# Optimization experiments

Measured on AMD Instinct MI355X. Metric: run time of the kernel, lower is better.

The kernel has to match this reference:

```python
import jax, jax.numpy as jnp
import numpy as np


def _ln(x, g, b, eps=1e-5):
    m = jnp.mean(x, axis=-1, keepdims=True)
    v = jnp.mean((x - m) ** 2, axis=-1, keepdims=True)
    return (x - m) / jnp.sqrt(v + eps) * g + b


def _win_part(x, ws):
    # (B,H,W,C) -> (B*nW, ws*ws, C)
    B, H, W, C = x.shape
    x = x.reshape(B, H // ws, ws, W // ws, ws, C)
    x = jnp.transpose(x, (0, 1, 3, 2, 4, 5))
    return x.reshape(-1, ws * ws, C)


def _win_rev(w, ws, H, W):
    # (B*nW, ws, ws, C) -> (B,H,W,C)
    C = w.shape[-1]
    B = w.shape[0] // ((H // ws) * (W // ws))
    x = w.reshape(B, H // ws, W // ws, ws, ws, C)
    x = jnp.transpose(x, (0, 1, 3, 2, 4, 5))
    return x.reshape(B, H, W, C)


def _build_mask(H, W, ws, ss):
    # standard Swin SW-MSA mask, built with numpy at trace time (static shapes)
    img = np.zeros((H, W), np.float32)
    cnt = 0
    for hs in (slice(0, -ws), slice(-ws, -ss), slice(-ss, None)):
        for wsl in (slice(0, -ws), slice(-ws, -ss), slice(-ss, None)):
            img[hs, wsl] = cnt
            cnt += 1
    mw = img.reshape(H // ws, ws, W // ws, ws).transpose(0, 2, 1, 3).reshape(-1, ws * ws)
    diff = mw[:, None, :] - mw[:, :, None]  # (nW, N, N)
    return jnp.asarray(np.where(diff != 0, -np.inf, 0.0).astype(np.float32))


def _swin_block(x, H, W, ws, shift, heads, p):
    B, L, C = x.shape
    hd = C // heads
    N = ws * ws
    shortcut = x
    xg = _ln(x, p['ln1_g'], p['ln1_b']).reshape(B, H, W, C)
    mask = None
    if shift > 0:
        xg = jnp.roll(xg, shift=(-shift, -shift), axis=(1, 2))
        mask = _build_mask(H, W, ws, shift)
    xw = _win_part(xg, ws)  # (B_, N, C)
    qkv = xw @ p['qkv_w'] + p['qkv_b']  # (B_, N, 3C)
    qkv = jnp.transpose(qkv.reshape(-1, N, 3, heads, hd), (2, 0, 3, 1, 4))
    q, k, v = qkv[0] * (hd ** -0.5), qkv[1], qkv[2]  # (B_, h, N, hd)
    attn = jnp.einsum('bhnd,bhmd->bhnm', q, k)
    if mask is not None:
        nW = mask.shape[0]
        attn = attn.reshape(B, nW, heads, N, N) + mask[None, :, None]
        attn = attn.reshape(-1, heads, N, N)
    attn = jax.nn.softmax(attn, axis=-1)
    out = jnp.einsum('bhnm,bhmd->bhnd', attn, v)
    out = jnp.transpose(out, (0, 2, 1, 3)).reshape(-1, N, C)
    out = out @ p['proj_w'] + p['proj_b']
    xg = _win_rev(out.reshape(-1, ws, ws, C), ws, H, W)
    if shift > 0:
        xg = jnp.roll(xg, shift=(shift, shift), axis=(1, 2))
    x = shortcut + xg.reshape(B, L, C)
    h = jax.nn.gelu(_ln(x, p['ln2_g'], p['ln2_b']) @ p['fc1_w'] + p['fc1_b'], approximate=False)
    return x + (h @ p['fc2_w'] + p['fc2_b'])


def _patch_merge(x, H, W, g, b, w):
    B, L, C = x.shape
    xg = x.reshape(B, H, W, C)
    xc = jnp.concatenate([xg[:, 0::2, 0::2], xg[:, 1::2, 0::2], xg[:, 0::2, 1::2], xg[:, 1::2, 1::2]], axis=-1)
    xc = xc.reshape(B, (H // 2) * (W // 2), 4 * C)
    return _ln(xc, g, b) @ w


def setup_inputs() -> dict:
    key = jax.random.key(0)
    ks = jax.random.split(key, 16)
    B, H, W, C = 8, 96, 96, 128
    s = 0.02
    d = {'x': jax.random.normal(ks[0], (B, H * W, C), jnp.float32)}
    i = 1
    for pre in ('a_', 'b_'):
        d[pre + 'ln1_g'] = jnp.ones((C,), jnp.float32)
        d[pre + 'ln1_b'] = jnp.zeros((C,), jnp.float32)
        d[pre + 'qkv_w'] = s * jax.random.normal(ks[i], (C, 3 * C), jnp.float32); i += 1
        d[pre + 'qkv_b'] = jnp.zeros((3 * C,), jnp.float32)
        d[pre + 'proj_w'] = s * jax.random.normal(ks[i], (C, C), jnp.float32); i += 1
        d[pre + 'proj_b'] = jnp.zeros((C,), jnp.float32)
        d[pre + 'ln2_g'] = jnp.ones((C,), jnp.float32)
        d[pre + 'ln2_b'] = jnp.zeros((C,), jnp.float32)
        d[pre + 'fc1_w'] = s * jax.random.normal(ks[i], (C, 4 * C), jnp.float32); i += 1
        d[pre + 'fc1_b'] = jnp.zeros((4 * C,), jnp.float32)
        d[pre + 'fc2_w'] = s * jax.random.normal(ks[i], (4 * C, C), jnp.float32); i += 1
        d[pre + 'fc2_b'] = jnp.zeros((C,), jnp.float32)
    d['mln_g'] = jnp.ones((4 * C,), jnp.float32)
    d['mln_b'] = jnp.zeros((4 * C,), jnp.float32)
    d['red_w'] = s * jax.random.normal(ks[i], (4 * C, 2 * C), jnp.float32)
    d['H'] = H
    d['W'] = W
    return d


def reference(x, a_ln1_g, a_ln1_b, a_qkv_w, a_qkv_b, a_proj_w, a_proj_b, a_ln2_g, a_ln2_b, a_fc1_w, a_fc1_b, a_fc2_w, a_fc2_b, b_ln1_g, b_ln1_b, b_qkv_w, b_qkv_b, b_proj_w, b_proj_b, b_ln2_g, b_ln2_b, b_fc1_w, b_fc1_b, b_fc2_w, b_fc2_b, mln_g, mln_b, red_w, H, W):
    heads, ws = 4, 8
    pa = dict(ln1_g=a_ln1_g, ln1_b=a_ln1_b, qkv_w=a_qkv_w, qkv_b=a_qkv_b, proj_w=a_proj_w, proj_b=a_proj_b, ln2_g=a_ln2_g, ln2_b=a_ln2_b, fc1_w=a_fc1_w, fc1_b=a_fc1_b, fc2_w=a_fc2_w, fc2_b=a_fc2_b)
    pb = dict(ln1_g=b_ln1_g, ln1_b=b_ln1_b, qkv_w=b_qkv_w, qkv_b=b_qkv_b, proj_w=b_proj_w, proj_b=b_proj_b, ln2_g=b_ln2_g, ln2_b=b_ln2_b, fc1_w=b_fc1_w, fc1_b=b_fc1_b, fc2_w=b_fc2_w, fc2_b=b_fc2_b)
    x = _swin_block(x, H, W, ws, 0, heads, pa)          # W-MSA
    x = _swin_block(x, H, W, ws, ws // 2, heads, pb)     # SW-MSA
    return _patch_merge(x, H, W, mln_g, mln_b, red_w)    # (B, HW/4, 2C)
```

## Files before the change

### kernel.cpp

```cpp
#include <hip/hip_runtime.h>
#include <hip/hip_bf16.h>

typedef __bf16 bf16_t;
typedef __bf16 bf16x2 __attribute__((ext_vector_type(2)));
typedef __bf16 bf16x8 __attribute__((ext_vector_type(8)));
typedef float floatx4 __attribute__((ext_vector_type(4)));

#define NTOK 73728
#define LNS 136

__device__ __forceinline__ void gl16(const bf16_t* g, bf16_t* l) {
    __builtin_amdgcn_global_load_lds((const __attribute__((address_space(1))) void*)g,
                                     (__attribute__((address_space(3))) void*)l, 16, 0, 0);
}

__device__ __forceinline__ void stage_ln(const float* __restrict__ src, const float* __restrict__ g,
                                         const float* __restrict__ bta, bf16_t* lnA, int tid) {
    int r = tid >> 2, q = tid & 3;
    const float* rowp = src + (size_t)r * 128 + q * 32;
    float4 v[8];
    float s = 0.0f, sq = 0.0f;
    #pragma unroll
    for (int i = 0; i < 8; i++) {
        v[i] = *(const float4*)(rowp + i * 4);
        s += v[i].x + v[i].y + v[i].z + v[i].w;
        sq += v[i].x * v[i].x + v[i].y * v[i].y + v[i].z * v[i].z + v[i].w * v[i].w;
    }
    s += __shfl_xor(s, 1, 64); sq += __shfl_xor(sq, 1, 64);
    s += __shfl_xor(s, 2, 64); sq += __shfl_xor(sq, 2, 64);
    float m = s * (1.0f / 128.0f);
    float inv = rsqrtf(sq * (1.0f / 128.0f) - m * m + 1e-5f);
    bf16_t* dst = lnA + r * LNS + q * 32;
    #pragma unroll
    for (int i = 0; i < 4; i++) {
        float4 a = v[2 * i], b = v[2 * i + 1];
        float4 g0 = *(const float4*)(g + q * 32 + i * 8);
        float4 g1 = *(const float4*)(g + q * 32 + i * 8 + 4);
        float4 b0 = *(const float4*)(bta + q * 32 + i * 8);
        float4 b1 = *(const float4*)(bta + q * 32 + i * 8 + 4);
        bf16x8 o;
        o[0] = (bf16_t)((a.x - m) * inv * g0.x + b0.x);
        o[1] = (bf16_t)((a.y - m) * inv * g0.y + b0.y);
        o[2] = (bf16_t)((a.z - m) * inv * g0.z + b0.z);
        o[3] = (bf16_t)((a.w - m) * inv * g0.w + b0.w);
        o[4] = (bf16_t)((b.x - m) * inv * g1.x + b1.x);
        o[5] = (bf16_t)((b.y - m) * inv * g1.y + b1.y);
        o[6] = (bf16_t)((b.z - m) * inv * g1.z + b1.z);
        o[7] = (bf16_t)((b.w - m) * inv * g1.w + b1.w);
        *(bf16x8*)(dst + i * 8) = o;
    }
}

struct TPack {
    const float* src[9];
    bf16_t* dst[9];
    int K[9], N[9];
};
__global__ __launch_bounds__(256) void kconv_frag(TPack p) {
    int seg = blockIdx.y;
    int K = p.K[seg], N = p.N[seg];
    int idx = blockIdx.x * 256 + threadIdx.x;
    if (idx >= K * N) return;
    int j = idx & 7;
    int lane = (idx >> 3) & 63;
    int blk = idx >> 9;
    int tilesK = K >> 5;
    int ntile = blk / tilesK, kc = blk - ntile * tilesK;
    int n = ntile * 16 + (lane & 15);
    int k = kc * 32 + (lane >> 4) * 8 + j;
    p.dst[seg][idx] = (bf16_t)p.src[seg][(size_t)k * N + n];
}

__global__ __launch_bounds__(256, 4) void kqkv(const float* __restrict__ X,
                                               const float* __restrict__ g, const float* __restrict__ bta,
                                               const bf16_t* __restrict__ Wf,
                                               const float* __restrict__ bias,
                                               bf16_t* __restrict__ out) {
    alignas(16) __shared__ bf16_t lA[64 * LNS];
    const int tid = threadIdx.x;
    const int rowA = blockIdx.y * 64;
    const int rowB = blockIdx.x * 128;
    stage_ln(X + (size_t)rowA * 128, g, bta, lA, tid);
    __syncthreads();
    const int lane = tid & 63, wv = tid >> 6;
    const int frow = lane & 15, fq = lane >> 4;
    const bf16_t* pw = Wf + (size_t)((rowB >> 4) + wv * 2) * 4 * 512 + lane * 8;
    floatx4 acc[4][2] = {};
    #pragma unroll
    for (int kc = 0; kc < 4; kc++) {
        bf16x8 af[4], bfr[2];
        #pragma unroll
        for (int j = 0; j < 2; j++)
            bfr[j] = *(const bf16x8*)(pw + (size_t)(j * 4 + kc) * 512);
        #pragma unroll
        for (int i = 0; i < 4; i++)
            af[i] = *(const bf16x8*)&lA[(i * 16 + frow) * LNS + kc * 32 + fq * 8];
        #pragma unroll
        for (int i = 0; i < 4; i++)
            #pragma unroll
            for (int j = 0; j < 2; j++)
                acc[i][j] = __builtin_amdgcn_mfma_f32_16x16x32_bf16(af[i], bfr[j], acc[i][j], 0, 0, 0);
    }
    #pragma unroll
    for (int j = 0; j < 2; j++) {
        int col = rowB + wv * 32 + j * 16 + frow;
        float bs = bias[col];
        #pragma unroll
        for (int i = 0; i < 4; i++)
            #pragma unroll
            for (int r = 0; r < 4; r++) {
                int row = rowA + i * 16 + fq * 4 + r;
                out[(size_t)row * 384 + col] = (bf16_t)(acc[i][j][r] + bs);
            }
    }
}

__global__ __launch_bounds__(256, 4) void kfused(const bf16_t* __restrict__ attn,
                                                 const bf16_t* __restrict__ Wpf,
                                                 const float* __restrict__ bp,
                                                 const float* __restrict__ resin,
                                                 float* __restrict__ resout,
                                                 const float* __restrict__ g, const float* __restrict__ bta,
                                                 const bf16_t* __restrict__ W1f,
                                                 const float* __restrict__ b1,
                                                 const bf16_t* __restrict__ W2f,
                                                 const float* __restrict__ b2) {
    alignas(16) __shared__ bf16_t lA[64 * LNS];
    alignas(16) __shared__ bf16_t lH[64 * LNS];
    __shared__ float psum[4 * 64], psq[4 * 64];
    const int tid = threadIdx.x;
    const int rowA = blockIdx.x * 64;
    const int lane = tid & 63, wv = tid >> 6;
    const int frow = lane & 15, fq = lane >> 4;

    {
        const int sr = tid >> 2, sc = (tid & 3) * 8;
        const bf16_t* pa = attn + (size_t)(rowA + sr) * 128 + sc;
        gl16(pa,      &lA[tid * 8]);
        gl16(pa + 32, &lA[2048 + tid * 8]);
        gl16(pa + 64, &lA[4096 + tid * 8]);
        gl16(pa + 96, &lA[6144 + tid * 8]);
    }
    __syncthreads();

    floatx4 accP[4][2] = {};
    {
        const bf16_t* pw = Wpf + (size_t)(wv * 2) * 4 * 512 + lane * 8;
        #pragma unroll
        for (int kc = 0; kc < 4; kc++) {
            bf16x8 af[4], bfr[2];
            #pragma unroll
            for (int j = 0; j < 2; j++)
                bfr[j] = *(const bf16x8*)(pw + (size_t)(j * 4 + kc) * 512);
            #pragma unroll
            for (int i = 0; i < 4; i++)
                af[i] = *(const bf16x8*)&lA[kc * 2048 + (i * 16 + frow) * 32 + fq * 8];
            #pragma unroll
            for (int i = 0; i < 4; i++)
                #pragma unroll
                for (int j = 0; j < 2; j++)
                    accP[i][j] = __builtin_amdgcn_mfma_f32_16x16x32_bf16(af[i], bfr[j], accP[i][j], 0, 0, 0);
        }
    }

    {
        float bs0 = bp[wv * 32 + frow];
        float bs1 = bp[wv * 32 + 16 + frow];
        #pragma unroll
        for (int i = 0; i < 4; i++) {
            #pragma unroll
            for (int r = 0; r < 4; r++) {
                int row = i * 16 + fq * 4 + r;
                size_t off = (size_t)(rowA + row) * 128 + wv * 32 + frow;
                float v0 = resin[off] + accP[i][0][r] + bs0;
                float v1 = resin[off + 16] + accP[i][1][r] + bs1;
                resout[off] = v0;
                resout[off + 16] = v1;
                float s = v0 + v1, sq = v0 * v0 + v1 * v1;
                #pragma unroll
                for (int d = 1; d < 16; d <<= 1) { s += __shfl_xor(s, d, 64); sq += __shfl_xor(sq, d, 64); }
                if (frow == 0) { psum[wv * 64 + row] = s; psq[wv * 64 + row] = sq; }
            }
        }
    }
    __syncthreads();

    {
        int r = tid >> 2, q = tid & 3;
        float s  = psum[r] + psum[64 + r] + psum[128 + r] + psum[192 + r];
        float sq = psq[r]  + psq[64 + r]  + psq[128 + r]  + psq[192 + r];
        float m = s * (1.0f / 128.0f);
        float inv = rsqrtf(sq * (1.0f / 128.0f) - m * m + 1e-5f);
        const float* rowp = resout + (size_t)(rowA + r) * 128 + q * 32;
        bf16_t* dst = lA + r * LNS + q * 32;
        #pragma unroll
        for (int i = 0; i < 4; i++) {
            float4 a = *(const float4*)(rowp + i * 8);
            float4 b = *(const float4*)(rowp + i * 8 + 4);
            float4 g0 = *(const float4*)(g + q * 32 + i * 8);
            float4 g1 = *(const float4*)(g + q * 32 + i * 8 + 4);
            float4 b0 = *(const float4*)(bta + q * 32 + i * 8);
            float4 b1 = *(const float4*)(bta + q * 32 + i * 8 + 4);
            bf16x8 o;
            o[0] = (bf16_t)((a.x - m) * inv * g0.x + b0.x);
            o[1] = (bf16_t)((a.y - m) * inv * g0.y + b0.y);
            o[2] = (bf16_t)((a.z - m) * inv * g0.z + b0.z);
            o[3] = (bf16_t)((a.w - m) * inv * g0.w + b0.w);
            o[4] = (bf16_t)((b.x - m) * inv * g1.x + b1.x);
            o[5] = (bf16_t)((b.y - m) * inv * g1.y + b1.y);
            o[6] = (bf16_t)((b.z - m) * inv * g1.z + b1.z);
            o[7] = (bf16_t)((b.w - m) * inv * g1.w + b1.w);
            *(bf16x8*)(dst + i * 8) = o;
        }
    }
    __syncthreads();

    const bf16_t* pw1 = W1f + lane * 8;
    const bf16_t* pw2 = W2f + lane * 8;
    floatx4 accO[4][2] = {};
    for (int cn = 0; cn < 4; cn++) {
        floatx4 accH[4][2] = {};
        #pragma unroll
        for (int kc = 0; kc < 4; kc++) {
            bf16x8 af[4], bfr[2];
            #pragma unroll
            for (int j = 0; j < 2; j++)
                bfr[j] = *(const bf16x8*)(pw1 + (size_t)((cn * 8 + wv * 2 + j) * 4 + kc) * 512);
            #pragma unroll
            for (int i = 0; i < 4; i++)
                af[i] = *(const bf16x8*)&lA[(i * 16 + frow) * LNS + kc * 32 + fq * 8];
            #pragma unroll
            for (int i = 0; i < 4; i++)
                #pragma unroll
                for (int j = 0; j < 2; j++)
                    accH[i][j] = __builtin_amdgcn_mfma_f32_16x16x32_bf16(af[i], bfr[j], accH[i][j], 0, 0, 0);
        }
        #pragma unroll
        for (int j = 0; j < 2; j++) {
            int col = wv * 32 + j * 16 + frow;
            float bs = b1[cn * 128 + col];
            #pragma unroll
            for (int i = 0; i < 4; i++)
                #pragma unroll
                for (int r = 0; r < 4; r++) {
                    int row = i * 16 + fq * 4 + r;
                    float v = accH[i][j][r] + bs;
                    float u = 1.5957691216057308f * (v + 0.044715f * v * v * v);
                    lH[row * LNS + col] = (bf16_t)(v / (1.0f + __expf(-u)));
                }
        }
        __syncthreads();
        #pragma unroll
        for (int kc = 0; kc < 4; kc++) {
            bf16x8 af[4], bfr[2];
            #pragma unroll
            for (int j = 0; j < 2; j++)
                bfr[j] = *(const bf16x8*)(pw2 + (size_t)((wv * 2 + j) * 16 + cn * 4 + kc) * 512);
            #pragma unroll
            for (int i = 0; i < 4; i++)
                af[i] = *(const bf16x8*)&lH[(i * 16 + frow) * LNS + kc * 32 + fq * 8];
            #pragma unroll
            for (int i = 0; i < 4; i++)
                #pragma unroll
                for (int j = 0; j < 2; j++)
                    accO[i][j] = __builtin_amdgcn_mfma_f32_16x16x32_bf16(af[i], bfr[j], accO[i][j], 0, 0, 0);
        }
        __syncthreads();
    }

    #pragma unroll
    for (int j = 0; j < 2; j++) {
        int col = wv * 32 + j * 16 + frow;
        float bs = b2[col];
        #pragma unroll
        for (int i = 0; i < 4; i++)
            #pragma unroll
            for (int r = 0; r < 4; r++) {
                int row = rowA + i * 16 + fq * 4 + r;
                size_t off = (size_t)row * 128 + col;
                resout[off] = resout[off] + accO[i][j][r] + bs;
            }
    }
}

__global__ __launch_bounds__(256, 4) void gemmred(const bf16_t* __restrict__ A,
                                                  const bf16_t* __restrict__ Bf,
                                                  float* __restrict__ outf,
                                                  int M, int N, int K) {
    alignas(16) __shared__ bf16_t lA[2 * 64 * 32];
    const int tid = threadIdx.x;
    const int lane = tid & 63;
    const int wv = tid >> 6;
    const int wm = (wv & 1) * 32;
    const int wn = (wv >> 1) * 64;
    const int frow = lane & 15, fq = lane >> 4;
    const int rowA = blockIdx.y * 64;
    const int rowB = blockIdx.x * 128;
    const int sr = tid >> 2, sc = (tid & 3) * 8;
    const int tilesK = K >> 5;
    const bf16_t* pa = A + (size_t)(rowA + sr) * K + sc;
    const bf16_t* pb = Bf + (size_t)((rowB + wn) >> 4) * tilesK * 512 + lane * 8;
    floatx4 acc[2][4] = {};
    for (int k0 = 0; k0 < K; k0 += 64) {
        __syncthreads();
        gl16(pa + k0,      &lA[tid * 8]);
        gl16(pa + k0 + 32, &lA[2048 + tid * 8]);
        __syncthreads();
        #pragma unroll
        for (int s = 0; s < 2; s++) {
            int kcg = (k0 >> 5) + s;
            bf16x8 af[2], bfr[4];
            #pragma unroll
            for (int j = 0; j < 4; j++)
                bfr[j] = *(const bf16x8*)(pb + (size_t)(j * tilesK + kcg) * 512);
            #pragma unroll
            for (int i = 0; i < 2; i++)
                af[i] = *(const bf16x8*)&lA[s * 2048 + (wm + i * 16 + frow) * 32 + fq * 8];
            #pragma unroll
            for (int i = 0; i < 2; i++)
                #pragma unroll
                for (int j = 0; j < 4; j++)
                    acc[i][j] = __builtin_amdgcn_mfma_f32_16x16x32_bf16(af[i], bfr[j], acc[i][j], 0, 0, 0);
        }
    }
    #pragma unroll
    for (int i = 0; i < 2; i++)
        #pragma unroll
        for (int j = 0; j < 4; j++) {
            int col = rowB + wn + j * 16 + frow;
            #pragma unroll
            for (int r = 0; r < 4; r++) {
                int row = rowA + wm + i * 16 + fq * 4 + r;
                outf[(size_t)row * N + col] = acc[i][j][r];
            }
        }
}

__global__ __launch_bounds__(256) void kmergeln(const float* __restrict__ x, const float* __restrict__ g,
                                                const float* __restrict__ bta, bf16_t* __restrict__ out) {
    int row = blockIdx.x * 4 + (threadIdx.x >> 6);
    int lane = threadIdx.x & 63;
    int b = row / 2304; int rr = row - b * 2304;
    int i2 = rr / 48, j2 = rr - i2 * 48;
    int q = lane >> 4;
    int cc = (lane & 15) * 8;
    int di = q & 1, dj = q >> 1;
    int src = ((b * 96 + i2 * 2 + di) * 96 + (j2 * 2 + dj)) * 128 + cc;
    float4 a0 = *(const float4*)&x[src];
    float4 a1 = *(const float4*)&x[src + 4];
    float s  = a0.x + a0.y + a0.z + a0.w + a1.x + a1.y + a1.z + a1.w;
    float sq = a0.x*a0.x + a0.y*a0.y + a0.z*a0.z + a0.w*a0.w
             + a1.x*a1.x + a1.y*a1.y + a1.z*a1.z + a1.w*a1.w;
    #pragma unroll
    for (int d = 1; d < 64; d <<= 1) { s += __shfl_xor(s, d, 64); sq += __shfl_xor(sq, d, 64); }
    float m = s * (1.0f / 512.0f);
    float var = sq * (1.0f / 512.0f) - m * m;
    float inv = 1.0f / sqrtf(var + 1e-5f);
    int c = q * 128 + cc;
    float4 g0 = *(const float4*)&g[c];
    float4 g1 = *(const float4*)&g[c + 4];
    float4 b0 = *(const float4*)&bta[c];
    float4 b1 = *(const float4*)&bta[c + 4];
    bf16x8 o;
    o[0] = (bf16_t)((a0.x - m) * inv * g0.x + b0.x);
    o[1] = (bf16_t)((a0.y - m) * inv * g0.y + b0.y);
    o[2] = (bf16_t)((a0.z - m) * inv * g0.z + b0.z);
    o[3] = (bf16_t)((a0.w - m) * inv * g0.w + b0.w);
    o[4] = (bf16_t)((a1.x - m) * inv * g1.x + b1.x);
    o[5] = (bf16_t)((a1.y - m) * inv * g1.y + b1.y);
    o[6] = (bf16_t)((a1.z - m) * inv * g1.z + b1.z);
    o[7] = (bf16_t)((a1.w - m) * inv * g1.w + b1.w);
    *(bf16x8*)&out[row * 512 + c] = o;
}

__global__ __launch_bounds__(64) void kattn(const bf16_t* __restrict__ qkv, bf16_t* __restrict__ out, int shift) {
    alignas(16) __shared__ bf16_t lp[64 * 64];
    alignas(16) __shared__ bf16_t lv[64 * 32];
    int blk = blockIdx.x;
    int win = blk >> 2, h = blk & 3;
    int b = win / 144; int wr = win - b * 144;
    int wi = wr / 12, wj = wr - wi * 12;
    int ri0 = wi * 8, rj0 = wj * 8;
    int lane = threadIdx.x;
    auto trow = [&](int n) {
        int oi = ri0 + (n >> 3) + shift; oi = (oi >= 96) ? oi - 96 : oi;
        int oj = rj0 + (n & 7) + shift;  oj = (oj >= 96) ? oj - 96 : oj;
        return (b * 96 + oi) * 96 + oj;
    };
    {
        size_t base = (size_t)trow(lane) * 384 + 256 + h * 32;
        *(uint4*)&lv[lane * 32]      = *(const uint4*)&qkv[base];
        *(uint4*)&lv[lane * 32 + 8]  = *(const uint4*)&qkv[base + 8];
        *(uint4*)&lv[lane * 32 + 16] = *(const uint4*)&qkv[base + 16];
        *(uint4*)&lv[lane * 32 + 24] = *(const uint4*)&qkv[base + 24];
    }
    int frow = lane & 15, fk = (lane >> 4) * 8;
    bf16x8 qf[4], kf[4];
    #pragma unroll
    for (int t = 0; t < 4; t++) {
        size_t rq = (size_t)trow(t * 16 + frow) * 384;
        qf[t] = *(const bf16x8*)&qkv[rq + h * 32 + fk];
        kf[t] = *(const bf16x8*)&qkv[rq + 128 + h * 32 + fk];
    }
    floatx4 S[4][4] = {};
    #pragma unroll
    for (int mt = 0; mt < 4; mt++)
        #pragma unroll
        for (int nt = 0; nt < 4; nt++)
            S[mt][nt] = __builtin_amdgcn_mfma_f32_16x16x32_bf16(qf[mt], kf[nt], S[mt][nt], 0, 0, 0);
    const float scale = 0.17677669529663687f;
    #pragma unroll
    for (int mt = 0; mt < 4; mt++)
        #pragma unroll
        for (int nt = 0; nt < 4; nt++)
            #pragma unroll
            for (int r = 0; r < 4; r++) S[mt][nt][r] *= scale;
    if (shift > 0) {
        auto grpn = [&](int n) {
            int ri = ri0 + (n >> 3), rj = rj0 + (n & 7);
            int gr = (ri < 88) ? 0 : ((ri < 92) ? 1 : 2);
            int gc = (rj < 88) ? 0 : ((rj < 92) ? 1 : 2);
            return gr * 3 + gc;
        };
        int gk[4];
        #pragma unroll
        for (int nt = 0; nt < 4; nt++) gk[nt] = grpn(nt * 16 + frow);
        #pragma unroll
        for (int mt = 0; mt < 4; mt++)
            #pragma unroll
            for (int r = 0; r < 4; r++) {
                int gq = grpn(mt * 16 + (lane >> 4) * 4 + r);
                #pragma unroll
                for (int nt = 0; nt < 4; nt++)
                    if (gq != gk[nt]) S[mt][nt][r] = -1e30f;
            }
    }
    #pragma unroll
    for (int mt = 0; mt < 4; mt++) {
        #pragma unroll
        for (int r = 0; r < 4; r++) {
            float mx = fmaxf(fmaxf(S[mt][0][r], S[mt][1][r]), fmaxf(S[mt][2][r], S[mt][3][r]));
            #pragma unroll
            for (int d = 1; d < 16; d <<= 1) mx = fmaxf(mx, __shfl_xor(mx, d, 64));
            float sm = 0.0f;
            #pragma unroll
            for (int nt = 0; nt < 4; nt++) {
                float p = __expf(S[mt][nt][r] - mx);
                S[mt][nt][r] = p;
                sm += p;
            }
            #pragma unroll
            for (int d = 1; d < 16; d <<= 1) sm += __shfl_xor(sm, d, 64);
            float inv = 1.0f / sm;
            #pragma unroll
            for (int nt = 0; nt < 4; nt++) S[mt][nt][r] *= inv;
        }
    }
    #pragma unroll
    for (int mt = 0; mt < 4; mt++)
        #pragma unroll
        for (int nt = 0; nt < 4; nt++)
            #pragma unroll
            for (int r = 0; r < 4; r++)
                lp[(mt * 16 + (lane >> 4) * 4 + r) * 64 + nt * 16 + frow] = (bf16_t)S[mt][nt][r];
    __syncthreads();
    floatx4 O[4][2] = {};
    #pragma unroll
    for (int ks = 0; ks < 2; ks++) {
        bf16x8 vbs[2];
        #pragma unroll
        for (int nt = 0; nt < 2; nt++)
            #pragma unroll
            for (int j = 0; j < 8; j++)
                vbs[nt][j] = lv[(ks * 32 + fk + j) * 32 + nt * 16 + frow];
        #pragma unroll
        for (int mt = 0; mt < 4; mt++) {
            bf16x8 pa = *(const bf16x8*)&lp[(mt * 16 + frow) * 64 + ks * 32 + fk];
            #pragma unroll
            for (int nt = 0; nt < 2; nt++)
                O[mt][nt] = __builtin_amdgcn_mfma_f32_16x16x32_bf16(pa, vbs[nt], O[mt][nt], 0, 0, 0);
        }
    }
    #pragma unroll
    for (int mt = 0; mt < 4; mt++) {
        #pragma unroll
        for (int r = 0; r < 4; r++) {
            int qr = mt * 16 + (lane >> 4) * 4 + r;
            size_t orow = (size_t)trow(qr) * 128 + h * 32;
            #pragma unroll
            for (int nt = 0; nt < 2; nt++)
                out[orow + nt * 16 + frow] = (bf16_t)O[mt][nt][r];
        }
    }
}

extern "C" void kernel_launch(void* const* d_in, const int* in_sizes, int n_in,
                              void* d_out, int out_size, void* d_ws, size_t ws_size,
                              hipStream_t stream) {
    const float* x       = (const float*)d_in[0];
    const float* a_ln1g  = (const float*)d_in[1];
    const float* a_ln1b  = (const float*)d_in[2];
    const float* a_qkvw  = (const float*)d_in[3];
    const float* a_qkvb  = (const float*)d_in[4];
    const float* a_projw = (const float*)d_in[5];
    const float* a_projb = (const float*)d_in[6];
    const float* a_ln2g  = (const float*)d_in[7];
    const float* a_ln2b  = (const float*)d_in[8];
    const float* a_fc1w  = (const float*)d_in[9];
    const float* a_fc1b  = (const float*)d_in[10];
    const float* a_fc2w  = (const float*)d_in[11];
    const float* a_fc2b  = (const float*)d_in[12];
    const float* b_ln1g  = (const float*)d_in[13];
    const float* b_ln1b  = (const float*)d_in[14];
    const float* b_qkvw  = (const float*)d_in[15];
    const float* b_qkvb  = (const float*)d_in[16];
    const float* b_projw = (const float*)d_in[17];
    const float* b_projb = (const float*)d_in[18];
    const float* b_ln2g  = (const float*)d_in[19];
    const float* b_ln2b  = (const float*)d_in[20];
    const float* b_fc1w  = (const float*)d_in[21];
    const float* b_fc1b  = (const float*)d_in[22];
    const float* b_fc2w  = (const float*)d_in[23];
    const float* b_fc2b  = (const float*)d_in[24];
    const float* mlng    = (const float*)d_in[25];
    const float* mlnb    = (const float*)d_in[26];
    const float* redw    = (const float*)d_in[27];
    float* out = (float*)d_out;

    char* p = (char*)d_ws;
    float*  buf_x   = (float*)p;  p += (size_t)NTOK * 128 * 4;
    bf16_t* buf_qkv = (bf16_t*)p; p += (size_t)NTOK * 384 * 2;
    bf16_t* buf_attn= (bf16_t*)p; p += (size_t)NTOK * 128 * 2;
    bf16_t* buf_mrg = (bf16_t*)p; p += (size_t)18432 * 512 * 2;
    bf16_t* wt      = (bf16_t*)p;
    bf16_t* aqkvF  = wt;
    bf16_t* aprojF = aqkvF  + 384 * 128;
    bf16_t* afc1F  = aprojF + 128 * 128;
    bf16_t* afc2F  = afc1F  + 512 * 128;
    bf16_t* bqkvF  = afc2F  + 128 * 512;
    bf16_t* bprojF = bqkvF  + 384 * 128;
    bf16_t* bfc1F  = bprojF + 128 * 128;
    bf16_t* bfc2F  = bfc1F  + 512 * 128;
    bf16_t* redF   = bfc2F  + 128 * 512;

    TPack tp;
    const float* srcs[9] = {a_qkvw, a_projw, a_fc1w, a_fc2w, b_qkvw, b_projw, b_fc1w, b_fc2w, redw};
    bf16_t* dsts[9] = {aqkvF, aprojF, afc1F, afc2F, bqkvF, bprojF, bfc1F, bfc2F, redF};
    int Ks[9] = {128, 128, 128, 512, 128, 128, 128, 512, 512};
    int Ns[9] = {384, 128, 512, 128, 384, 128, 512, 128, 256};
    for (int i = 0; i < 9; i++) { tp.src[i] = srcs[i]; tp.dst[i] = dsts[i]; tp.K[i] = Ks[i]; tp.N[i] = Ns[i]; }
    kconv_frag<<<dim3(512, 9), dim3(256), 0, stream>>>(tp);

    const dim3 blk256(256);
    const int MG = NTOK / 64;

    kqkv<<<dim3(3, MG), blk256, 0, stream>>>(x, a_ln1g, a_ln1b, aqkvF, a_qkvb, buf_qkv);
    kattn<<<dim3(1152 * 4), dim3(64), 0, stream>>>(buf_qkv, buf_attn, 0);
    kfused<<<dim3(MG), blk256, 0, stream>>>(buf_attn, aprojF, a_projb, x, buf_x,
                                            a_ln2g, a_ln2b, afc1F, a_fc1b, afc2F, a_fc2b);

    kqkv<<<dim3(3, MG), blk256, 0, stream>>>(buf_x, b_ln1g, b_ln1b, bqkvF, b_qkvb, buf_qkv);
    kattn<<<dim3(1152 * 4), dim3(64), 0, stream>>>(buf_qkv, buf_attn, 4);
    kfused<<<dim3(MG), blk256, 0, stream>>>(buf_attn, bprojF, b_projb, buf_x, buf_x,
                                            b_ln2g, b_ln2b, bfc1F, b_fc1b, bfc2F, b_fc2b);

    kmergeln<<<dim3(18432 / 4), blk256, 0, stream>>>(buf_x, mlng, mlnb, buf_mrg);
    gemmred<<<dim3(2, 288), blk256, 0, stream>>>(buf_mrg, redF, out, 18432, 256, 512);
}
```

Measured before the change: 457.0 us.

## Compute all QKV columns per block and keep residual in registers in fused MLP

The QKV kernel now loops over all three 128-column chunks inside one block, so the layernorm of each 64-row tile is staged once instead of three times. The fused proj/MLP kernel keeps the post-attention residual in registers and computes LN2 directly from them, instead of writing it to global memory and reading it back twice. This cuts global traffic and repeated LN work, but raises register pressure (launch bounds lowered to 3 blocks per SM) and gives the QKV launch a third as many blocks.

```diff
diff --git a/kernel.cpp b/kernel.cpp
--- a/kernel.cpp
+++ b/kernel.cpp
@@ -78,44 +78,45 @@
                                                bf16_t* __restrict__ out) {
     alignas(16) __shared__ bf16_t lA[64 * LNS];
     const int tid = threadIdx.x;
-    const int rowA = blockIdx.y * 64;
-    const int rowB = blockIdx.x * 128;
+    const int rowA = blockIdx.x * 64;
     stage_ln(X + (size_t)rowA * 128, g, bta, lA, tid);
     __syncthreads();
     const int lane = tid & 63, wv = tid >> 6;
     const int frow = lane & 15, fq = lane >> 4;
-    const bf16_t* pw = Wf + (size_t)((rowB >> 4) + wv * 2) * 4 * 512 + lane * 8;
-    floatx4 acc[4][2] = {};
-    #pragma unroll
-    for (int kc = 0; kc < 4; kc++) {
-        bf16x8 af[4], bfr[2];
-        #pragma unroll
-        for (int j = 0; j < 2; j++)
-            bfr[j] = *(const bf16x8*)(pw + (size_t)(j * 4 + kc) * 512);
-        #pragma unroll
-        for (int i = 0; i < 4; i++)
-            af[i] = *(const bf16x8*)&lA[(i * 16 + frow) * LNS + kc * 32 + fq * 8];
-        #pragma unroll
-        for (int i = 0; i < 4; i++)
+    const bf16_t* pw = Wf + lane * 8;
+    for (int cn = 0; cn < 3; cn++) {
+        floatx4 acc[4][2] = {};
+        #pragma unroll
+        for (int kc = 0; kc < 4; kc++) {
+            bf16x8 af[4], bfr[2];
             #pragma unroll
             for (int j = 0; j < 2; j++)
-                acc[i][j] = __builtin_amdgcn_mfma_f32_16x16x32_bf16(af[i], bfr[j], acc[i][j], 0, 0, 0);
-    }
-    #pragma unroll
-    for (int j = 0; j < 2; j++) {
-        int col = rowB + wv * 32 + j * 16 + frow;
-        float bs = bias[col];
-        #pragma unroll
-        for (int i = 0; i < 4; i++)
-            #pragma unroll
-            for (int r = 0; r < 4; r++) {
-                int row = rowA + i * 16 + fq * 4 + r;
-                out[(size_t)row * 384 + col] = (bf16_t)(acc[i][j][r] + bs);
-            }
-    }
-}
-
-__global__ __launch_bounds__(256, 4) void kfused(const bf16_t* __restrict__ attn,
+                bfr[j] = *(const bf16x8*)(pw + (size_t)((cn * 8 + wv * 2 + j) * 4 + kc) * 512);
+            #pragma unroll
+            for (int i = 0; i < 4; i++)
+                af[i] = *(const bf16x8*)&lA[(i * 16 + frow) * LNS + kc * 32 + fq * 8];
+            #pragma unroll
+            for (int i = 0; i < 4; i++)
+                #pragma unroll
+                for (int j = 0; j < 2; j++)
+                    acc[i][j] = __builtin_amdgcn_mfma_f32_16x16x32_bf16(af[i], bfr[j], acc[i][j], 0, 0, 0);
+        }
+        #pragma unroll
+        for (int j = 0; j < 2; j++) {
+            int col = cn * 128 + wv * 32 + j * 16 + frow;
+            float bs = bias[col];
+            #pragma unroll
+            for (int i = 0; i < 4; i++)
+                #pragma unroll
+                for (int r = 0; r < 4; r++) {
+                    int row = rowA + i * 16 + fq * 4 + r;
+                    out[(size_t)row * 384 + col] = (bf16_t)(acc[i][j][r] + bs);
+                }
+        }
+    }
+}
+
+__global__ __launch_bounds__(256, 3) void kfused(const bf16_t* __restrict__ attn,
                                                  const bf16_t* __restrict__ Wpf,
                                                  const float* __restrict__ bp,
                                                  const float* __restrict__ resin,
@@ -174,8 +175,8 @@
                 size_t off = (size_t)(rowA + row) * 128 + wv * 32 + frow;
                 float v0 = resin[off] + accP[i][0][r] + bs0;
                 float v1 = resin[off + 16] + accP[i][1][r] + bs1;
-                resout[off] = v0;
-                resout[off + 16] = v1;
+                accP[i][0][r] = v0;
+                accP[i][1][r] = v1;
                 float s = v0 + v1, sq = v0 * v0 + v1 * v1;
                 #pragma unroll
                 for (int d = 1; d < 16; d <<= 1) { s += __shfl_xor(s, d, 64); sq += __shfl_xor(sq, d, 64); }
@@ -186,31 +187,20 @@
     __syncthreads();
 
     {
-        int r = tid >> 2, q = tid & 3;
-        float s  = psum[r] + psum[64 + r] + psum[128 + r] + psum[192 + r];
-        float sq = psq[r]  + psq[64 + r]  + psq[128 + r]  + psq[192 + r];
-        float m = s * (1.0f / 128.0f);
-        float inv = rsqrtf(sq * (1.0f / 128.0f) - m * m + 1e-5f);
-        const float* rowp = resout + (size_t)(rowA + r) * 128 + q * 32;
-        bf16_t* dst = lA + r * LNS + q * 32;
+        float g0 = g[wv * 32 + frow],      b0 = bta[wv * 32 + frow];
+        float g1 = g[wv * 32 + 16 + frow], b1v = bta[wv * 32 + 16 + frow];
         #pragma unroll
         for (int i = 0; i < 4; i++) {
-            float4 a = *(const float4*)(rowp + i * 8);
-            float4 b = *(const float4*)(rowp + i * 8 + 4);
-            float4 g0 = *(const float4*)(g + q * 32 + i * 8);
-            float4 g1 = *(const float4*)(g + q * 32 + i * 8 + 4);
-            float4 b0 = *(const float4*)(bta + q * 32 + i * 8);
-            float4 b1 = *(const float4*)(bta + q * 32 + i * 8 + 4);
-            bf16x8 o;
-            o[0] = (bf16_t)((a.x - m) * inv * g0.x + b0.x);
-            o[1] = (bf16_t)((a.y - m) * inv * g0.y + b0.y);
-            o[2] = (bf16_t)((a.z - m) * inv * g0.z + b0.z);
-            o[3] = (bf16_t)((a.w - m) * inv * g0.w + b0.w);
-            o[4] = (bf16_t)((b.x - m) * inv * g1.x + b1.x);
-            o[5] = (bf16_t)((b.y - m) * inv * g1.y + b1.y);
-            o[6] = (bf16_t)((b.z - m) * inv * g1.z + b1.z);
-            o[7] = (bf16_t)((b.w - m) * inv * g1.w + b1.w);
-            *(bf16x8*)(dst + i * 8) = o;
+            #pragma unroll
+            for (int r = 0; r < 4; r++) {
+                int row = i * 16 + fq * 4 + r;
+                float s  = psum[row] + psum[64 + row] + psum[128 + row] + psum[192 + row];
+                float sq = psq[row]  + psq[64 + row]  + psq[128 + row]  + psq[192 + row];
+                float m = s * (1.0f / 128.0f);
+                float inv = rsqrtf(sq * (1.0f / 128.0f) - m * m + 1e-5f);
+                lA[row * LNS + wv * 32 + frow]      = (bf16_t)((accP[i][0][r] - m) * inv * g0 + b0);
+                lA[row * LNS + wv * 32 + 16 + frow] = (bf16_t)((accP[i][1][r] - m) * inv * g1 + b1v);
+            }
         }
     }
     __syncthreads();
@@ -277,8 +267,7 @@
             #pragma unroll
             for (int r = 0; r < 4; r++) {
                 int row = rowA + i * 16 + fq * 4 + r;
-                size_t off = (size_t)row * 128 + col;
-                resout[off] = resout[off] + accO[i][j][r] + bs;
+                resout[(size_t)row * 128 + col] = accP[i][j][r] + accO[i][j][r] + bs;
             }
     }
 }
@@ -554,12 +543,12 @@
     const dim3 blk256(256);
     const int MG = NTOK / 64;
 
-    kqkv<<<dim3(3, MG), blk256, 0, stream>>>(x, a_ln1g, a_ln1b, aqkvF, a_qkvb, buf_qkv);
+    kqkv<<<dim3(MG), blk256, 0, stream>>>(x, a_ln1g, a_ln1b, aqkvF, a_qkvb, buf_qkv);
     kattn<<<dim3(1152 * 4), dim3(64), 0, stream>>>(buf_qkv, buf_attn, 0);
     kfused<<<dim3(MG), blk256, 0, stream>>>(buf_attn, aprojF, a_projb, x, buf_x,
                                             a_ln2g, a_ln2b, afc1F, a_fc1b, afc2F, a_fc2b);
 
-    kqkv<<<dim3(3, MG), blk256, 0, stream>>>(buf_x, b_ln1g, b_ln1b, bqkvF, b_qkvb, buf_qkv);
+    kqkv<<<dim3(MG), blk256, 0, stream>>>(buf_x, b_ln1g, b_ln1b, bqkvF, b_qkvb, buf_qkv);
     kattn<<<dim3(1152 * 4), dim3(64), 0, stream>>>(buf_qkv, buf_attn, 4);
     kfused<<<dim3(MG), blk256, 0, stream>>>(buf_attn, bprojF, b_projb, buf_x, buf_x,
                                             b_ln2g, b_ln2b, bfc1F, b_fc1b, bfc2F, b_fc2b);
```

After: 405.8 us. 11.2% less time.
